# Performance work log

Hardware: AMD Instinct MI355X
Metric: run time of the kernel (lower is better)

## Reference

```python
import jax, jax.numpy as jnp
import numpy as np
from jax import lax

NEG = -1e30  # log-domain 'zero'

B, T, D, V, L = 32, 800, 512, 1024, 100  # batch, frames, eprojs, odim, max label len


def setup_inputs() -> dict:
    key = jax.random.key(0)
    k0, k1, k2, k3, k4 = jax.random.split(key, 5)
    hpad = jax.random.normal(k0, (B, T, D), jnp.float32)
    W = jax.random.normal(k1, (V, D), jnp.float32) / np.sqrt(D).astype(np.float32)
    b = jnp.zeros((V,), jnp.float32)
    labels = jax.random.randint(k2, (B, L), 1, V, dtype=jnp.int32)  # blank=0 excluded
    ilens = jax.random.randint(k3, (B,), T // 2, T + 1, dtype=jnp.int32)
    label_lens = jax.random.randint(k4, (B,), L // 2, L + 1, dtype=jnp.int32)
    return {"hpad": hpad, "W": W, "b": b, "labels": labels,
            "ilens": ilens, "label_lens": label_lens}


def _ctc_loss(hpad, W, b, labels, ilens, label_lens):
    # ctc_lo: Linear(eprojs, odim); dropout_rate=0 -> identity
    logits = jnp.einsum('btd,vd->btv', hpad, W) + b          # [B,T,V]
    logp = jax.nn.log_softmax(logits, axis=-1)               # warp_ctc softmaxes acts internally
    Bb, Tt, Vv = logits.shape
    Ll = labels.shape[1]
    S = 2 * Ll + 1
    # extended label sequence with interleaved blanks (blank id = 0)
    ext = jnp.zeros((Bb, S), jnp.int32).at[:, 1::2].set(labels)  # [B,S]
    # gather log-probs of extended labels: [B,T,S] -> [T,B,S]
    lp_ext = jnp.take_along_axis(logp, jnp.broadcast_to(ext[:, None, :], (Bb, Tt, S)), axis=2)
    lp_seq = jnp.transpose(lp_ext, (1, 0, 2))                # [T,B,S]
    # skip transition s-2 -> s allowed iff ext[s] != blank and ext[s] != ext[s-2]
    ext_m2 = jnp.pad(ext, ((0, 0), (2, 0)))[:, :S]
    allow = (jnp.arange(S)[None, :] >= 2) & (ext != 0) & (ext != ext_m2)  # [B,S]

    # alpha init at t=0: positions 0 (blank) and 1 (first label)
    a0 = jnp.full((Bb, S), NEG, logp.dtype)
    a0 = a0.at[:, 0].set(lp_seq[0][:, 0])
    first = jnp.where(label_lens > 0, lp_seq[0][:, 1], NEG)
    a0 = a0.at[:, 1].set(first)

    def step(alpha, inp):
        lp_t, t = inp
        p1 = jnp.concatenate([jnp.full((Bb, 1), NEG, alpha.dtype), alpha[:, :-1]], axis=1)
        p2 = jnp.concatenate([jnp.full((Bb, 2), NEG, alpha.dtype), alpha[:, :-2]], axis=1)
        c = jnp.logaddexp(alpha, p1)
        c = jnp.where(allow, jnp.logaddexp(c, p2), c)
        new = c + lp_t
        active = (t < ilens)[:, None]  # frames past ilen leave alpha unchanged
        return jnp.where(active, new, alpha), None

    alphaT, _ = lax.scan(step, a0, (lp_seq[1:], jnp.arange(1, Tt)))

    idx_last = (2 * label_lens).astype(jnp.int32)            # ext index of final blank
    last = jnp.take_along_axis(alphaT, idx_last[:, None], axis=1)[:, 0]
    prev = jnp.take_along_axis(alphaT, jnp.maximum(idx_last - 1, 0)[:, None], axis=1)[:, 0]
    ll = jnp.logaddexp(last, jnp.where(label_lens > 0, prev, NEG))
    costs = -ll                                              # per-utterance NLL
    return jnp.sum(costs) / Bb                               # chainer-like: sum / batch


def reference(hpad, W, b, labels, ilens, label_lens):
    return _ctc_loss(hpad, W, b, labels, ilens, label_lens)
```

## Files before the change

kernel.cpp:

```cpp
#include <hip/hip_runtime.h>
#include <hip/hip_bf16.h>
#include <cstdint>

constexpr int CBATCH = 32;
constexpr int CT = 800;
constexpr int CD = 512;
constexpr int CV = 1024;
constexpr int CL = 100;
constexpr int CM = CBATCH * CT;
constexpr int CS = 2 * CL + 1;
constexpr int CSPL = 256;
constexpr float NEGV = -1e30f;
constexpr float INV_LN2 = 1.4426950408889634f;
constexpr float LN2F = 0.6931471805599453f;

typedef __bf16 bf16x8 __attribute__((ext_vector_type(8)));
typedef float f32x4 __attribute__((ext_vector_type(4)));
typedef unsigned short ushort8 __attribute__((ext_vector_type(8)));

__device__ inline unsigned short f2bf(float f) {
  union { float f; unsigned u; } v; v.f = f;
  unsigned u = v.u;
  unsigned r = (u + 0x7fffu + ((u >> 16) & 1u)) >> 16;
  return (unsigned short)r;
}
__device__ inline float bf2f(unsigned short u) {
  unsigned x = (unsigned)u << 16;
  return __builtin_bit_cast(float, x);
}
__device__ inline float bitf(int x) { return __builtin_bit_cast(float, x); }

__device__ inline float fexp2(float x) { return __builtin_amdgcn_exp2f(x); }
__device__ inline float flog2(float x) { return __builtin_amdgcn_logf(x); }

__device__ inline float dpp_shr1(float x, float fill) {
  int r = __builtin_amdgcn_update_dpp(__builtin_bit_cast(int, fill),
                                      __builtin_bit_cast(int, x),
                                      0x138, 0xF, 0xF, false);
  return __builtin_bit_cast(float, r);
}
__device__ inline int dpp_shr1_int(int x, int fill) {
  return __builtin_amdgcn_update_dpp(fill, x, 0x138, 0xF, 0xF, false);
}
__device__ inline float dpp_shl1(float x, float fill) {
  int r = __builtin_amdgcn_update_dpp(__builtin_bit_cast(int, fill),
                                      __builtin_bit_cast(int, x),
                                      0x130, 0xF, 0xF, false);
  return __builtin_bit_cast(float, r);
}
__device__ inline int dpp_shl1_int(int x, int fill) {
  return __builtin_amdgcn_update_dpp(fill, x, 0x130, 0xF, 0xF, false);
}

__device__ inline void gload_lds16(const void* g, void* l) {
  __builtin_amdgcn_global_load_lds(
      (const __attribute__((address_space(1))) unsigned int*)g,
      (__attribute__((address_space(3))) unsigned int*)l, 16, 0, 0);
}

__global__ void cvt_kernel(const float* __restrict__ in, unsigned short* __restrict__ out, int n4) {
  int i = blockIdx.x * blockDim.x + threadIdx.x;
  if (i < n4) {
    float4 v = reinterpret_cast<const float4*>(in)[i];
    ushort4 o;
    o.x = f2bf(v.x); o.y = f2bf(v.y); o.z = f2bf(v.z); o.w = f2bf(v.w);
    reinterpret_cast<ushort4*>(out)[i] = o;
  }
}

constexpr int GBK = 64;

__global__ __launch_bounds__(256, 2) void gemm_kernel(
    const unsigned short* __restrict__ A,
    const unsigned short* __restrict__ Bt,
    const float* __restrict__ bias,
    unsigned short* __restrict__ C)
{
  __shared__ __align__(16) unsigned short As[128 * GBK];
  __shared__ __align__(16) unsigned short Bs[128 * GBK];
  const int tid = threadIdx.x;
  const int lane = tid & 63;
  const int wave = tid >> 6;
  const int wr = wave >> 1, wc = wave & 1;
  const int bm = blockIdx.x, bn = blockIdx.y;

  f32x4 acc[4][4] = {};

  for (int k0 = 0; k0 < CD; k0 += GBK) {
#pragma unroll
    for (int i = 0; i < 4; ++i) {
      int c = tid + 256 * i;
      int row = c >> 3;
      int scol = ((c & 7) ^ (row & 7)) * 8;
      gload_lds16(&A[(size_t)(bm * 128 + row) * CD + k0 + scol], &As[c * 8]);
      gload_lds16(&Bt[(size_t)(bn * 128 + row) * CD + k0 + scol], &Bs[c * 8]);
    }
    __syncthreads();
#pragma unroll
    for (int kk = 0; kk < 2; ++kk) {
      bf16x8 af[4], bfr[4];
#pragma unroll
      for (int m = 0; m < 4; ++m) {
        int row = wr * 64 + m * 16 + (lane & 15);
        int cb = kk * 4 + (lane >> 4);
        af[m] = *reinterpret_cast<const bf16x8*>(
            &As[row * GBK + (cb ^ (row & 7)) * 8]);
      }
#pragma unroll
      for (int n = 0; n < 4; ++n) {
        int row = wc * 64 + n * 16 + (lane & 15);
        int cb = kk * 4 + (lane >> 4);
        bfr[n] = *reinterpret_cast<const bf16x8*>(
            &Bs[row * GBK + (cb ^ (row & 7)) * 8]);
      }
#pragma unroll
      for (int m = 0; m < 4; ++m)
#pragma unroll
        for (int n = 0; n < 4; ++n)
          acc[m][n] = __builtin_amdgcn_mfma_f32_16x16x32_bf16(af[m], bfr[n], acc[m][n], 0, 0, 0);
    }
    __syncthreads();
  }

  float bv[4];
#pragma unroll
  for (int n = 0; n < 4; ++n)
    bv[n] = bias[bn * 128 + wc * 64 + n * 16 + (lane & 15)];
#pragma unroll
  for (int m = 0; m < 4; ++m) {
    int rbase = bm * 128 + wr * 64 + m * 16 + (lane >> 4) * 4;
#pragma unroll
    for (int n = 0; n < 4; ++n) {
      int col = bn * 128 + wc * 64 + n * 16 + (lane & 15);
#pragma unroll
      for (int r = 0; r < 4; ++r)
        C[(size_t)(rbase + r) * CV + col] = f2bf(acc[m][n][r] + bv[n]);
    }
  }
}

__global__ void lse_gather_kernel(const unsigned short* __restrict__ C,
                                  const int* __restrict__ labels,
                                  float* __restrict__ lpg) {
  const int wave = threadIdx.x >> 6, lane = threadIdx.x & 63;
  const int row = blockIdx.x * 4 + wave;
  const int b = row / CT;
  const unsigned short* p = C + (size_t)row * CV;
  ushort8 v0 = reinterpret_cast<const ushort8*>(p)[lane * 2];
  ushort8 v1 = reinterpret_cast<const ushort8*>(p)[lane * 2 + 1];
  float f[16];
#pragma unroll
  for (int i = 0; i < 8; ++i) { f[i] = bf2f(v0[i]); f[8 + i] = bf2f(v1[i]); }
  float m = f[0];
#pragma unroll
  for (int i = 1; i < 16; ++i) m = fmaxf(m, f[i]);
#pragma unroll
  for (int off = 32; off >= 1; off >>= 1) m = fmaxf(m, __shfl_xor(m, off));
  float s = 0.f;
#pragma unroll
  for (int i = 0; i < 16; ++i) s += __expf(f[i] - m);
#pragma unroll
  for (int off = 32; off >= 1; off >>= 1) s += __shfl_xor(s, off);
  const float l = m + __logf(s);

  float4 o;
  if (lane < 51) {
    const int* lab = labels + b * CL;
    const int s0 = lane * 4;
    float vals[4];
#pragma unroll
    for (int j = 0; j < 4; ++j) {
      int st = s0 + j;
      if (st >= CS) { vals[j] = NEGV; continue; }
      int e = (st & 1) ? lab[st >> 1] : 0;
      vals[j] = (bf2f(p[e]) - l) * INV_LN2;
    }
    o.x = fexp2(vals[0]); o.y = fexp2(vals[1]);
    o.z = fexp2(vals[2]); o.w = fexp2(vals[3]);
  } else {
    o.x = o.y = o.z = o.w = 0.f;
  }
  reinterpret_cast<float4*>(lpg + (size_t)row * CSPL)[lane] = o;
}

constexpr int RRING = 64;
constexpr int NCHUNKS = 51;

__global__ __launch_bounds__(256, 1) void ctc_kernel(
    const float* __restrict__ lpg, const int* __restrict__ labels,
    const int* __restrict__ ilens, const int* __restrict__ llens,
    float* __restrict__ abuf, int* __restrict__ kbuf) {
  __shared__ __align__(16) float ring[RRING * CSPL];
  __shared__ int ready[NCHUNKS + 1];
  __shared__ int done;
  const int bq = blockIdx.x;
  const int b = bq >> 1, dir = bq & 1;
  const int tid = threadIdx.x;
  const int lane = tid & 63;
  const int wid = tid >> 6;
  const float* base = lpg + (size_t)b * CT * CSPL;

  for (int i = tid; i < NCHUNKS + 1; i += 256) ready[i] = 0;
  if (tid == 0) done = 0;
  __syncthreads();

  if (wid == 0) {
    const int ilen = ilens[b];
    const int ll = llens[b];
    const int* lab = labels + b * CL;
    const int s0 = lane * 4;
    float m1f = 0.f, m3f = 0.f;
    if (lane < 51) {
      int s1 = s0 + 1;
      if (s1 >= 3 && s1 < CS && lab[s1 >> 1] != lab[(s1 >> 1) - 1]) m1f = 1.f;
      int s3 = s0 + 3;
      if (s3 < CS && lab[s3 >> 1] != lab[(s3 >> 1) - 1]) m3f = 1.f;
    }
    float a0, a1, a2, a3;
    int kk = 0;
    if (dir == 0) {
      f32x4 r0 = reinterpret_cast<const f32x4*>(base)[lane];
      a0 = (lane == 0) ? r0[0] : 0.f;
      a1 = (lane == 0 && ll > 0) ? r0[1] : 0.f;
      a2 = 0.f; a3 = 0.f;
    } else {
      const int e1 = 2 * ll, e2 = 2 * ll - 1;
      a0 = (s0 + 0 == e1 || s0 + 0 == e2) ? 1.f : 0.f;
      a1 = (s0 + 1 == e1 || s0 + 1 == e2) ? 1.f : 0.f;
      a2 = (s0 + 2 == e1 || s0 + 2 == e2) ? 1.f : 0.f;
      a3 = (s0 + 3 == e1 || s0 + 3 == e2) ? 1.f : 0.f;
    }

    volatile int* rdy = ready;
    while (rdy[0] == 0) {}
    asm volatile("" ::: "memory");
    f32x4 lpA = *reinterpret_cast<const f32x4*>(&ring[0 * CSPL + lane * 4]);
    f32x4 lpB = *reinterpret_cast<const f32x4*>(&ring[1 * CSPL + lane * 4]);
    f32x4 lpC = *reinterpret_cast<const f32x4*>(&ring[2 * CSPL + lane * 4]);
    f32x4 lpD = *reinterpret_cast<const f32x4*>(&ring[3 * CSPL + lane * 4]);
    f32x4 lpE = *reinterpret_cast<const f32x4*>(&ring[4 * CSPL + lane * 4]);
    f32x4 lpF = *reinterpret_cast<const f32x4*>(&ring[5 * CSPL + lane * 4]);
    f32x4 lpG = *reinterpret_cast<const f32x4*>(&ring[6 * CSPL + lane * 4]);
    f32x4 lpH = *reinterpret_cast<const f32x4*>(&ring[7 * CSPL + lane * 4]);

#define RENORM4                                                           \
      {                                                                   \
        float mm_ = fmaxf(fmaxf(a0, a1), fmaxf(a2, a3));                  \
        int e_ = (__builtin_bit_cast(int, mm_) >> 23) & 0xFF;             \
        float sc_ = bitf((254 - e_) << 23);                               \
        a0 *= sc_; a1 *= sc_; a2 *= sc_; a3 *= sc_;                       \
        kk = K_ + e_ - 127;                                               \
      }

#define FSTEP(LP, J)                                                      \
    {                                                                     \
      const int u_ = uc + (J);                                            \
      f32x4 cur_ = LP;                                                    \
      LP = *reinterpret_cast<const f32x4*>(                               \
          &ring[((u_ + 8) & (RRING - 1)) * CSPL + lane * 4]);             \
      float nm_ = dpp_shr1(a3, 0.f);                                      \
      int nk_ = dpp_shr1_int(kk, (int)0xE0000000);                        \
      if (1 + u_ < ilen) {                                                \
        int K_ = nk_ > kk ? nk_ : kk;                                     \
        int ta_ = kk - K_ + 127;                                          \
        int tn_ = nk_ - K_ + 127;                                         \
        float fa_ = ta_ > 0 ? bitf(ta_ << 23) : 0.f;                      \
        float fn_ = tn_ > 0 ? bitf(tn_ << 23) : 0.f;                      \
        float na3_ = nm_ * fn_;                                           \
        float c0_ = __builtin_fmaf(a0, fa_, na3_);                        \
        float c1_ = __builtin_fmaf(a0 + a1, fa_, na3_ * m1f);             \
        float c2_ = (a1 + a2) * fa_;                                      \
        float c3_ = __builtin_fmaf(a1, m3f, a2 + a3) * fa_;               \
        a0 = c0_ * cur_[0]; a1 = c1_ * cur_[1];                           \
        a2 = c2_ * cur_[2]; a3 = c3_ * cur_[3];                           \
        if (((J) & 3) == 3) { RENORM4 } else { kk = K_; }                 \
      }                                                                   \
    }

#define BSTEP(LP, J)                                                      \
    {                                                                     \
      const int u_ = uc + (J);                                            \
      const int r_ = 799 - u_;                                            \
      f32x4 q_ = LP;                                                      \
      LP = *reinterpret_cast<const f32x4*>(                               \
          &ring[((u_ + 8) & (RRING - 1)) * CSPL + lane * 4]);             \
      float g0_ = a0 * q_[0], g1_ = a1 * q_[1];                           \
      float g2_ = a2 * q_[2], g3_ = a3 * q_[3];                           \
      float h_ = __builtin_fmaf(g1_, m1f, g0_);                           \
      float hn_ = dpp_shl1(h_, 0.f);                                      \
      int nk_ = dpp_shl1_int(kk, (int)0xE0000000);                        \
      if (r_ > 400 && r_ < ilen) {                                        \
        int K_ = nk_ > kk ? nk_ : kk;                                     \
        int ta_ = kk - K_ + 127;                                          \
        int tn_ = nk_ - K_ + 127;                                         \
        float fa_ = ta_ > 0 ? bitf(ta_ << 23) : 0.f;                      \
        float fn_ = tn_ > 0 ? bitf(tn_ << 23) : 0.f;                      \
        float c0_ = (g0_ + g1_) * fa_;                                    \
        float c1_ = __builtin_fmaf(g3_, m3f, g1_ + g2_) * fa_;            \
        float c2_ = (g2_ + g3_) * fa_;                                    \
        float c3_ = __builtin_fmaf(hn_, fn_, g3_ * fa_);                  \
        a0 = c0_; a1 = c1_; a2 = c2_; a3 = c3_;                           \
        if (((J) & 3) == 3) { RENORM4 } else { kk = K_; }                 \
      }                                                                   \
    }

    if (dir == 0) {
      for (int c = 0; c < 50; ++c) {
        while (rdy[c] == 0) {}
        while (rdy[c + 1] == 0) {}
        asm volatile("" ::: "memory");
        const int uc = 8 * c;
        FSTEP(lpA, 0) FSTEP(lpB, 1) FSTEP(lpC, 2) FSTEP(lpD, 3)
        FSTEP(lpE, 4) FSTEP(lpF, 5) FSTEP(lpG, 6) FSTEP(lpH, 7)
        asm volatile("s_waitcnt lgkmcnt(0)" ::: "memory");
        if (lane == 0) *(volatile int*)&done = c + 1;
      }
    } else {
      for (int c = 0; c < 50; ++c) {
        while (rdy[c] == 0) {}
        while (rdy[c + 1] == 0) {}
        asm volatile("" ::: "memory");
        const int uc = 8 * c;
        BSTEP(lpA, 0) BSTEP(lpB, 1) BSTEP(lpC, 2) BSTEP(lpD, 3)
        BSTEP(lpE, 4) BSTEP(lpF, 5) BSTEP(lpG, 6) BSTEP(lpH, 7)
        asm volatile("s_waitcnt lgkmcnt(0)" ::: "memory");
        if (lane == 0) *(volatile int*)&done = c + 1;
      }
    }
#undef FSTEP
#undef BSTEP
#undef RENORM4

    const int idx = bq * 64 + lane;
    f32x4 mv; mv[0] = a0; mv[1] = a1; mv[2] = a2; mv[3] = a3;
    reinterpret_cast<f32x4*>(abuf)[idx] = mv;
    kbuf[idx] = kk;
  } else {
    const int p = wid - 1;
    for (int c = p; c < NCHUNKS; c += 3) {
      if (c >= 8) {
        while (*(volatile int*)&done < c - 7) {}
      }
      asm volatile("" ::: "memory");
      const int i0 = 8 * c;
      const float* src = base + (size_t)(dir ? (799 - i0) : (1 + i0)) * CSPL;
      const ptrdiff_t strd = dir ? -(ptrdiff_t)CSPL : (ptrdiff_t)CSPL;
      f32x4 v0 = reinterpret_cast<const f32x4*>(src + 0 * strd)[lane];
      f32x4 v1 = reinterpret_cast<const f32x4*>(src + 1 * strd)[lane];
      f32x4 v2 = reinterpret_cast<const f32x4*>(src + 2 * strd)[lane];
      f32x4 v3 = reinterpret_cast<const f32x4*>(src + 3 * strd)[lane];
      f32x4 v4 = reinterpret_cast<const f32x4*>(src + 4 * strd)[lane];
      f32x4 v5 = reinterpret_cast<const f32x4*>(src + 5 * strd)[lane];
      f32x4 v6 = reinterpret_cast<const f32x4*>(src + 6 * strd)[lane];
      f32x4 v7 = reinterpret_cast<const f32x4*>(src + 7 * strd)[lane];
      float* dst = &ring[((i0) & (RRING - 1)) * CSPL + lane * 4];
      *reinterpret_cast<f32x4*>(dst + 0 * CSPL) = v0;
      *reinterpret_cast<f32x4*>(dst + 1 * CSPL) = v1;
      *reinterpret_cast<f32x4*>(dst + 2 * CSPL) = v2;
      *reinterpret_cast<f32x4*>(dst + 3 * CSPL) = v3;
      *reinterpret_cast<f32x4*>(dst + 4 * CSPL) = v4;
      *reinterpret_cast<f32x4*>(dst + 5 * CSPL) = v5;
      *reinterpret_cast<f32x4*>(dst + 6 * CSPL) = v6;
      *reinterpret_cast<f32x4*>(dst + 7 * CSPL) = v7;
      asm volatile("s_waitcnt lgkmcnt(0)" ::: "memory");
      if (lane == 0) *(volatile int*)&ready[c] = 1;
    }
  }
}

__global__ void combine_kernel(const float* __restrict__ abuf,
                               const int* __restrict__ kbuf,
                               float* __restrict__ out) {
  const int b = blockIdx.x;
  const int lane = threadIdx.x;
  f32x4 am = reinterpret_cast<const f32x4*>(abuf)[(b * 2 + 0) * 64 + lane];
  f32x4 bm = reinterpret_cast<const f32x4*>(abuf)[(b * 2 + 1) * 64 + lane];
  int ak = kbuf[(b * 2 + 0) * 64 + lane];
  int bk = kbuf[(b * 2 + 1) * 64 + lane];
  float val = am[0] * bm[0] + am[1] * bm[1] + am[2] * bm[2] + am[3] * bm[3];
  int e = (val > 0.f) ? (ak + bk) : (int)0xC0000000;
  int E = e;
#pragma unroll
  for (int off = 32; off >= 1; off >>= 1) E = max(E, __shfl_xor(E, off));
  int t = e - E + 127;
  float f = t > 0 ? __builtin_bit_cast(float, t << 23) : 0.f;
  float c = val * f;
#pragma unroll
  for (int off = 32; off >= 1; off >>= 1) c += __shfl_xor(c, off);
  if (lane == 0) {
    float ll2 = flog2(c) + (float)E;
    atomicAdd(out, -ll2 * (LN2F / CBATCH));
  }
}

extern "C" void kernel_launch(void* const* d_in, const int* in_sizes, int n_in,
                              void* d_out, int out_size, void* d_ws, size_t ws_size,
                              hipStream_t stream) {
  const float* hpad = (const float*)d_in[0];
  const float* W    = (const float*)d_in[1];
  const float* bias = (const float*)d_in[2];
  const int* labels = (const int*)d_in[3];
  const int* ilens  = (const int*)d_in[4];
  const int* llens  = (const int*)d_in[5];
  float* out = (float*)d_out;

  char* ws = (char*)d_ws;
  size_t off = 0;
  auto alloc = [&](size_t bytes) -> void* {
    void* p = ws + off;
    off = (off + bytes + 255) & ~(size_t)255;
    return p;
  };
  unsigned short* Abf = (unsigned short*)alloc((size_t)CM * CD * 2);
  unsigned short* Wbf = (unsigned short*)alloc((size_t)CV * CD * 2);
  unsigned short* logits = (unsigned short*)alloc((size_t)CM * CV * 2);
  float* lpg  = (float*)alloc((size_t)(CM + 64) * CSPL * 4);
  float* abuf = (float*)alloc((size_t)CBATCH * 2 * 64 * 4 * sizeof(float));
  int*   kbuf = (int*)alloc((size_t)CBATCH * 2 * 64 * sizeof(int));

  hipMemsetAsync(d_out, 0, sizeof(float), stream);

  cvt_kernel<<<(CM * CD / 4 + 255) / 256, 256, 0, stream>>>(hpad, Abf, CM * CD / 4);
  cvt_kernel<<<(CV * CD / 4 + 255) / 256, 256, 0, stream>>>(W, Wbf, CV * CD / 4);
  gemm_kernel<<<dim3(CM / 128, CV / 128), 256, 0, stream>>>(Abf, Wbf, bias, logits);
  lse_gather_kernel<<<CM / 4, 256, 0, stream>>>(logits, labels, lpg);
  ctc_kernel<<<CBATCH * 2, 256, 0, stream>>>(lpg, labels, ilens, llens, abuf, kbuf);
  combine_kernel<<<CBATCH, 64, 0, stream>>>(abuf, kbuf, out);
}
```

Measured before the change: 113.2 us.

## Fuse log-softmax and label gather into CTC producer waves

Removes the standalone lse_gather kernel and its fp32 intermediate buffer. The CTC kernel's producer waves now read bf16 logits rows directly, compute the log-sum-exp and the extended-label probabilities, and write them into the shared ring. This saves a kernel launch and a large global write/read round trip. The risk is that producers, now limited to 64 blocks, may not keep pace with the serial recurrence.

Measured after the change: 231.1 us. 2.04x slower.

```diff
diff --git a/kernel.cpp b/kernel.cpp
--- a/kernel.cpp
+++ b/kernel.cpp
@@ -139,55 +139,11 @@
   }
 }
 
-__global__ void lse_gather_kernel(const unsigned short* __restrict__ C,
-                                  const int* __restrict__ labels,
-                                  float* __restrict__ lpg) {
-  const int wave = threadIdx.x >> 6, lane = threadIdx.x & 63;
-  const int row = blockIdx.x * 4 + wave;
-  const int b = row / CT;
-  const unsigned short* p = C + (size_t)row * CV;
-  ushort8 v0 = reinterpret_cast<const ushort8*>(p)[lane * 2];
-  ushort8 v1 = reinterpret_cast<const ushort8*>(p)[lane * 2 + 1];
-  float f[16];
-#pragma unroll
-  for (int i = 0; i < 8; ++i) { f[i] = bf2f(v0[i]); f[8 + i] = bf2f(v1[i]); }
-  float m = f[0];
-#pragma unroll
-  for (int i = 1; i < 16; ++i) m = fmaxf(m, f[i]);
-#pragma unroll
-  for (int off = 32; off >= 1; off >>= 1) m = fmaxf(m, __shfl_xor(m, off));
-  float s = 0.f;
-#pragma unroll
-  for (int i = 0; i < 16; ++i) s += __expf(f[i] - m);
-#pragma unroll
-  for (int off = 32; off >= 1; off >>= 1) s += __shfl_xor(s, off);
-  const float l = m + __logf(s);
-
-  float4 o;
-  if (lane < 51) {
-    const int* lab = labels + b * CL;
-    const int s0 = lane * 4;
-    float vals[4];
-#pragma unroll
-    for (int j = 0; j < 4; ++j) {
-      int st = s0 + j;
-      if (st >= CS) { vals[j] = NEGV; continue; }
-      int e = (st & 1) ? lab[st >> 1] : 0;
-      vals[j] = (bf2f(p[e]) - l) * INV_LN2;
-    }
-    o.x = fexp2(vals[0]); o.y = fexp2(vals[1]);
-    o.z = fexp2(vals[2]); o.w = fexp2(vals[3]);
-  } else {
-    o.x = o.y = o.z = o.w = 0.f;
-  }
-  reinterpret_cast<float4*>(lpg + (size_t)row * CSPL)[lane] = o;
-}
-
 constexpr int RRING = 64;
 constexpr int NCHUNKS = 51;
 
 __global__ __launch_bounds__(256, 1) void ctc_kernel(
-    const float* __restrict__ lpg, const int* __restrict__ labels,
+    const unsigned short* __restrict__ logits, const int* __restrict__ labels,
     const int* __restrict__ ilens, const int* __restrict__ llens,
     float* __restrict__ abuf, int* __restrict__ kbuf) {
   __shared__ __align__(16) float ring[RRING * CSPL];
@@ -198,7 +154,7 @@
   const int tid = threadIdx.x;
   const int lane = tid & 63;
   const int wid = tid >> 6;
-  const float* base = lpg + (size_t)b * CT * CSPL;
+  const int* lab = labels + b * CL;
 
   for (int i = tid; i < NCHUNKS + 1; i += 256) ready[i] = 0;
   if (tid == 0) done = 0;
@@ -207,7 +163,6 @@
   if (wid == 0) {
     const int ilen = ilens[b];
     const int ll = llens[b];
-    const int* lab = labels + b * CL;
     const int s0 = lane * 4;
     float m1f = 0.f, m3f = 0.f;
     if (lane < 51) {
@@ -219,9 +174,27 @@
     float a0, a1, a2, a3;
     int kk = 0;
     if (dir == 0) {
-      f32x4 r0 = reinterpret_cast<const f32x4*>(base)[lane];
-      a0 = (lane == 0) ? r0[0] : 0.f;
-      a1 = (lane == 0 && ll > 0) ? r0[1] : 0.f;
+      const unsigned short* prow = logits + (size_t)(b * CT) * CV;
+      ushort8 v0 = reinterpret_cast<const ushort8*>(prow)[lane * 2];
+      ushort8 v1 = reinterpret_cast<const ushort8*>(prow)[lane * 2 + 1];
+      float f[16];
+#pragma unroll
+      for (int q = 0; q < 8; ++q) { f[q] = bf2f(v0[q]); f[8 + q] = bf2f(v1[q]); }
+      float m = f[0];
+#pragma unroll
+      for (int q = 1; q < 16; ++q) m = fmaxf(m, f[q]);
+#pragma unroll
+      for (int off = 32; off >= 1; off >>= 1) m = fmaxf(m, __shfl_xor(m, off));
+      float s = 0.f;
+#pragma unroll
+      for (int q = 0; q < 16; ++q) s += __expf(f[q] - m);
+#pragma unroll
+      for (int off = 32; off >= 1; off >>= 1) s += __shfl_xor(s, off);
+      const float l = m + __logf(s);
+      float p0 = fexp2((bf2f(prow[0]) - l) * INV_LN2);
+      float p1 = fexp2((bf2f(prow[lab[0]]) - l) * INV_LN2);
+      a0 = (lane == 0) ? p0 : 0.f;
+      a1 = (lane == 0 && ll > 0) ? p1 : 0.f;
       a2 = 0.f; a3 = 0.f;
     } else {
       const int e1 = 2 * ll, e2 = 2 * ll - 1;
@@ -343,25 +316,44 @@
       }
       asm volatile("" ::: "memory");
       const int i0 = 8 * c;
-      const float* src = base + (size_t)(dir ? (799 - i0) : (1 + i0)) * CSPL;
-      const ptrdiff_t strd = dir ? -(ptrdiff_t)CSPL : (ptrdiff_t)CSPL;
-      f32x4 v0 = reinterpret_cast<const f32x4*>(src + 0 * strd)[lane];
-      f32x4 v1 = reinterpret_cast<const f32x4*>(src + 1 * strd)[lane];
-      f32x4 v2 = reinterpret_cast<const f32x4*>(src + 2 * strd)[lane];
-      f32x4 v3 = reinterpret_cast<const f32x4*>(src + 3 * strd)[lane];
-      f32x4 v4 = reinterpret_cast<const f32x4*>(src + 4 * strd)[lane];
-      f32x4 v5 = reinterpret_cast<const f32x4*>(src + 5 * strd)[lane];
-      f32x4 v6 = reinterpret_cast<const f32x4*>(src + 6 * strd)[lane];
-      f32x4 v7 = reinterpret_cast<const f32x4*>(src + 7 * strd)[lane];
-      float* dst = &ring[((i0) & (RRING - 1)) * CSPL + lane * 4];
-      *reinterpret_cast<f32x4*>(dst + 0 * CSPL) = v0;
-      *reinterpret_cast<f32x4*>(dst + 1 * CSPL) = v1;
-      *reinterpret_cast<f32x4*>(dst + 2 * CSPL) = v2;
-      *reinterpret_cast<f32x4*>(dst + 3 * CSPL) = v3;
-      *reinterpret_cast<f32x4*>(dst + 4 * CSPL) = v4;
-      *reinterpret_cast<f32x4*>(dst + 5 * CSPL) = v5;
-      *reinterpret_cast<f32x4*>(dst + 6 * CSPL) = v6;
-      *reinterpret_cast<f32x4*>(dst + 7 * CSPL) = v7;
+      for (int j = 0; j < 8; ++j) {
+        const int i = i0 + j;
+        const int rf = dir ? (799 - i) : (1 + i);
+        const unsigned short* prow = logits + (size_t)(b * CT + rf) * CV;
+        ushort8 v0 = reinterpret_cast<const ushort8*>(prow)[lane * 2];
+        ushort8 v1 = reinterpret_cast<const ushort8*>(prow)[lane * 2 + 1];
+        float f[16];
+#pragma unroll
+        for (int q = 0; q < 8; ++q) { f[q] = bf2f(v0[q]); f[8 + q] = bf2f(v1[q]); }
+        float m = f[0];
+#pragma unroll
+        for (int q = 1; q < 16; ++q) m = fmaxf(m, f[q]);
+#pragma unroll
+        for (int off = 32; off >= 1; off >>= 1) m = fmaxf(m, __shfl_xor(m, off));
+        float s = 0.f;
+#pragma unroll
+        for (int q = 0; q < 16; ++q) s += __expf(f[q] - m);
+#pragma unroll
+        for (int off = 32; off >= 1; off >>= 1) s += __shfl_xor(s, off);
+        const float l = m + __logf(s);
+        float4 o;
+        if (lane < 51) {
+          const int s0p = lane * 4;
+          float vals[4];
+#pragma unroll
+          for (int jj = 0; jj < 4; ++jj) {
+            int st = s0p + jj;
+            if (st >= CS) { vals[jj] = NEGV; continue; }
+            int e = (st & 1) ? lab[st >> 1] : 0;
+            vals[jj] = (bf2f(prow[e]) - l) * INV_LN2;
+          }
+          o.x = fexp2(vals[0]); o.y = fexp2(vals[1]);
+          o.z = fexp2(vals[2]); o.w = fexp2(vals[3]);
+        } else {
+          o.x = o.y = o.z = o.w = 0.f;
+        }
+        *reinterpret_cast<float4*>(&ring[(i & (RRING - 1)) * CSPL + lane * 4]) = o;
+      }
       asm volatile("s_waitcnt lgkmcnt(0)" ::: "memory");
       if (lane == 0) *(volatile int*)&ready[c] = 1;
     }
@@ -414,7 +406,6 @@
   unsigned short* Abf = (unsigned short*)alloc((size_t)CM * CD * 2);
   unsigned short* Wbf = (unsigned short*)alloc((size_t)CV * CD * 2);
   unsigned short* logits = (unsigned short*)alloc((size_t)CM * CV * 2);
-  float* lpg  = (float*)alloc((size_t)(CM + 64) * CSPL * 4);
   float* abuf = (float*)alloc((size_t)CBATCH * 2 * 64 * 4 * sizeof(float));
   int*   kbuf = (int*)alloc((size_t)CBATCH * 2 * 64 * sizeof(int));
 
@@ -423,7 +414,6 @@
   cvt_kernel<<<(CM * CD / 4 + 255) / 256, 256, 0, stream>>>(hpad, Abf, CM * CD / 4);
   cvt_kernel<<<(CV * CD / 4 + 255) / 256, 256, 0, stream>>>(W, Wbf, CV * CD / 4);
   gemm_kernel<<<dim3(CM / 128, CV / 128), 256, 0, stream>>>(Abf, Wbf, bias, logits);
-  lse_gather_kernel<<<CM / 4, 256, 0, stream>>>(logits, labels, lpg);
-  ctc_kernel<<<CBATCH * 2, 256, 0, stream>>>(lpg, labels, ilens, llens, abuf, kbuf);
+  ctc_kernel<<<CBATCH * 2, 256, 0, stream>>>(logits, labels, ilens, llens, abuf, kbuf);
   combine_kernel<<<CBATCH, 64, 0, stream>>>(abuf, kbuf, out);
 }
```
